# Kernel tuning notes

Measured on AMD Instinct MI355X. Metric: run time of the kernel, lower is better.

The kernel has to match this reference:

```python
import jax, jax.numpy as jnp
import numpy as np

N_TOKENS = 32768
INPUT_DIM = 1024
HIDDEN_DIM = 256
NUM_EXPERTS = 64
TOP_K = 2


def setup_inputs() -> dict:
    key = jax.random.key(0)
    kx, k1, k2, kb1, kb2 = jax.random.split(key, 5)
    # torch nn.Linear init scale ~ U(-1/sqrt(fan_in), 1/sqrt(fan_in)); use small normals
    x = jax.random.normal(kx, (N_TOKENS, INPUT_DIM), dtype=jnp.float32)
    w1 = jax.random.normal(k1, (HIDDEN_DIM, INPUT_DIM), dtype=jnp.float32) / np.sqrt(INPUT_DIM)
    b1 = jax.random.normal(kb1, (HIDDEN_DIM,), dtype=jnp.float32) * 0.01
    w2 = jax.random.normal(k2, (NUM_EXPERTS, HIDDEN_DIM), dtype=jnp.float32) / np.sqrt(HIDDEN_DIM)
    b2 = jax.random.normal(kb2, (NUM_EXPERTS,), dtype=jnp.float32) * 0.01
    return {"x": x, "w1": w1, "b1": b1, "w2": w2, "b2": b2}


def reference(x, w1, b1, w2, b2):
    # logits = Linear -> ReLU -> Linear
    h = jax.nn.relu(jnp.einsum("nd,hd->nh", x, w1) + b1)       # [N, hidden]
    logits = jnp.einsum("nh,eh->ne", h, w2) + b2               # [N, experts]
    top_k_logits, top_k_indices = jax.lax.top_k(logits, TOP_K)  # [N, k]
    top_k_gates = jax.nn.softmax(top_k_logits, axis=-1)
    return top_k_indices, top_k_gates
```

## Files before the change

### kernel.cpp

```cpp
#include <hip/hip_runtime.h>
#include <math.h>

#define N_TOK 32768
#define IN_DIM 1024
#define HID 256
#define NE 64

__global__ __launch_bounds__(256, 2)
void gemm1_relu(const float* __restrict__ x, const float* __restrict__ w1,
                const float* __restrict__ b1, float* __restrict__ h)
{
    __shared__ float Xs[32][72];
    __shared__ float Ws[32][256];

    const int tid = threadIdx.x;
    const int t0  = blockIdx.x * 64;
    const int tg  = tid >> 5;
    const int hg  = tid & 31;

    float acc[8][8];
    #pragma unroll
    for (int i = 0; i < 8; ++i)
        #pragma unroll
        for (int j = 0; j < 8; ++j) acc[i][j] = 0.f;

    for (int k0 = 0; k0 < IN_DIM; k0 += 32) {
        #pragma unroll
        for (int r = 0; r < 2; ++r) {
            int slot = tid + 256 * r;
            int t  = slot >> 3;
            int kq = (slot & 7) * 4;
            float4 v = *(const float4*)(x + (size_t)(t0 + t) * IN_DIM + k0 + kq);
            Xs[kq + 0][t] = v.x; Xs[kq + 1][t] = v.y;
            Xs[kq + 2][t] = v.z; Xs[kq + 3][t] = v.w;
        }
        #pragma unroll
        for (int r = 0; r < 8; ++r) {
            int slot = tid + 256 * r;
            int hh = slot >> 3;
            int kq = (slot & 7) * 4;
            float4 v = *(const float4*)(w1 + (size_t)hh * IN_DIM + k0 + kq);
            Ws[kq + 0][hh] = v.x; Ws[kq + 1][hh] = v.y;
            Ws[kq + 2][hh] = v.z; Ws[kq + 3][hh] = v.w;
        }
        __syncthreads();

        #pragma unroll
        for (int k = 0; k < 32; ++k) {
            float xv[8], wv[8];
            *(float4*)&xv[0] = *(const float4*)&Xs[k][tg * 8];
            *(float4*)&xv[4] = *(const float4*)&Xs[k][tg * 8 + 4];
            *(float4*)&wv[0] = *(const float4*)&Ws[k][hg * 8];
            *(float4*)&wv[4] = *(const float4*)&Ws[k][hg * 8 + 4];
            #pragma unroll
            for (int i = 0; i < 8; ++i)
                #pragma unroll
                for (int j = 0; j < 8; ++j)
                    acc[i][j] = fmaf(xv[i], wv[j], acc[i][j]);
        }
        __syncthreads();
    }

    float4 bv0 = *(const float4*)(b1 + hg * 8);
    float4 bv1 = *(const float4*)(b1 + hg * 8 + 4);
    float bias[8] = {bv0.x, bv0.y, bv0.z, bv0.w, bv1.x, bv1.y, bv1.z, bv1.w};
    #pragma unroll
    for (int i = 0; i < 8; ++i) {
        int t = t0 + tg * 8 + i;
        float4 o0, o1;
        o0.x = fmaxf(acc[i][0] + bias[0], 0.f);
        o0.y = fmaxf(acc[i][1] + bias[1], 0.f);
        o0.z = fmaxf(acc[i][2] + bias[2], 0.f);
        o0.w = fmaxf(acc[i][3] + bias[3], 0.f);
        o1.x = fmaxf(acc[i][4] + bias[4], 0.f);
        o1.y = fmaxf(acc[i][5] + bias[5], 0.f);
        o1.z = fmaxf(acc[i][6] + bias[6], 0.f);
        o1.w = fmaxf(acc[i][7] + bias[7], 0.f);
        *(float4*)(h + (size_t)t * HID + hg * 8)     = o0;
        *(float4*)(h + (size_t)t * HID + hg * 8 + 4) = o1;
    }
}

__global__ __launch_bounds__(256, 2)
void gemm2_topk(const float* __restrict__ h, const float* __restrict__ w2,
                const float* __restrict__ b2, float* __restrict__ out)
{
    __shared__ float Hs[32][72];
    __shared__ float W2s[32][64];
    __shared__ float Ls[64][65];

    const int tid = threadIdx.x;
    const int t0  = blockIdx.x * 64;
    const int tg  = tid >> 4;
    const int eg  = tid & 15;

    float acc[4][4];
    #pragma unroll
    for (int i = 0; i < 4; ++i)
        #pragma unroll
        for (int j = 0; j < 4; ++j) acc[i][j] = 0.f;

    for (int k0 = 0; k0 < HID; k0 += 32) {
        #pragma unroll
        for (int r = 0; r < 2; ++r) {
            int slot = tid + 256 * r;
            int t  = slot >> 3;
            int kq = (slot & 7) * 4;
            float4 v = *(const float4*)(h + (size_t)(t0 + t) * HID + k0 + kq);
            Hs[kq + 0][t] = v.x; Hs[kq + 1][t] = v.y;
            Hs[kq + 2][t] = v.z; Hs[kq + 3][t] = v.w;
        }
        #pragma unroll
        for (int r = 0; r < 2; ++r) {
            int slot = tid + 256 * r;
            int e  = slot >> 3;
            int kq = (slot & 7) * 4;
            float4 v = *(const float4*)(w2 + (size_t)e * HID + k0 + kq);
            W2s[kq + 0][e] = v.x; W2s[kq + 1][e] = v.y;
            W2s[kq + 2][e] = v.z; W2s[kq + 3][e] = v.w;
        }
        __syncthreads();

        #pragma unroll
        for (int k = 0; k < 32; ++k) {
            float hv[4], wv[4];
            *(float4*)&hv[0] = *(const float4*)&Hs[k][tg * 4];
            *(float4*)&wv[0] = *(const float4*)&W2s[k][eg * 4];
            #pragma unroll
            for (int i = 0; i < 4; ++i)
                #pragma unroll
                for (int j = 0; j < 4; ++j)
                    acc[i][j] = fmaf(hv[i], wv[j], acc[i][j]);
        }
        __syncthreads();
    }

    float4 b2v = *(const float4*)(b2 + eg * 4);
    float bb[4] = {b2v.x, b2v.y, b2v.z, b2v.w};
    #pragma unroll
    for (int i = 0; i < 4; ++i)
        #pragma unroll
        for (int j = 0; j < 4; ++j)
            Ls[tg * 4 + i][eg * 4 + j] = acc[i][j] + bb[j];
    __syncthreads();

    if (tid < 64) {
        const int t = tid;
        float m1 = -INFINITY, m2 = -INFINITY;
        int i1 = 0, i2 = 0;
        #pragma unroll 8
        for (int e = 0; e < NE; ++e) {
            float v = Ls[t][e];
            if (v > m1) { m2 = m1; i2 = i1; m1 = v; i1 = e; }
            else if (v > m2) { m2 = v; i2 = e; }
        }
        float e2  = expf(m2 - m1);
        float inv = 1.f / (1.f + e2);
        float g1  = inv;
        float g2  = e2 * inv;
        int gt = t0 + t;
        out[(size_t)gt * 2 + 0] = (float)i1;
        out[(size_t)gt * 2 + 1] = (float)i2;
        out[(size_t)2 * N_TOK + (size_t)gt * 2 + 0] = g1;
        out[(size_t)2 * N_TOK + (size_t)gt * 2 + 1] = g2;
    }
}

extern "C" void kernel_launch(void* const* d_in, const int* in_sizes, int n_in,
                              void* d_out, int out_size, void* d_ws, size_t ws_size,
                              hipStream_t stream) {
    const float* x  = (const float*)d_in[0];
    const float* w1 = (const float*)d_in[1];
    const float* b1 = (const float*)d_in[2];
    const float* w2 = (const float*)d_in[3];
    const float* b2 = (const float*)d_in[4];
    float* out = (float*)d_out;
    float* h   = (float*)d_ws;

    gemm1_relu<<<N_TOK / 64, 256, 0, stream>>>(x, w1, b1, h);
    gemm2_topk<<<N_TOK / 64, 256, 0, stream>>>(h, w2, b2, out);
}
```

Measured before the change: 417.8 us.

## Fuse both gating GEMMs and top-k into one kernel with swizzled LDS and prefetch

After: 556.4 us. 33.2% more time.

```diff
diff --git a/kernel.cpp b/kernel.cpp
--- a/kernel.cpp
+++ b/kernel.cpp
@@ -6,12 +6,18 @@
 #define HID 256
 #define NE 64
 
+union SMem {
+    struct { float Xs[32][64]; float Ws[32][256]; } a;
+    struct { float Hs[128][64]; float W2s[32][64]; } b;
+    float Ls[64][67];
+};
+
 __global__ __launch_bounds__(256, 2)
-void gemm1_relu(const float* __restrict__ x, const float* __restrict__ w1,
-                const float* __restrict__ b1, float* __restrict__ h)
+void moe_gate_fused(const float* __restrict__ x,  const float* __restrict__ w1,
+                    const float* __restrict__ b1, const float* __restrict__ w2,
+                    const float* __restrict__ b2, float* __restrict__ out)
 {
-    __shared__ float Xs[32][72];
-    __shared__ float Ws[32][256];
+    __shared__ SMem sm;
 
     const int tid = threadIdx.x;
     const int t0  = blockIdx.x * 64;
@@ -24,124 +30,162 @@
         #pragma unroll
         for (int j = 0; j < 8; ++j) acc[i][j] = 0.f;
 
-    for (int k0 = 0; k0 < IN_DIM; k0 += 32) {
+    float4 px[2], pw[8];
+    #pragma unroll
+    for (int r = 0; r < 2; ++r) {
+        int slot = tid + 256 * r;
+        int t = slot >> 3, kq = (slot & 7) * 4;
+        px[r] = *(const float4*)(x + (size_t)(t0 + t) * IN_DIM + kq);
+    }
+    #pragma unroll
+    for (int r = 0; r < 8; ++r) {
+        int slot = tid + 256 * r;
+        int hh = slot >> 3, kq = (slot & 7) * 4;
+        pw[r] = *(const float4*)(w1 + (size_t)hh * IN_DIM + kq);
+    }
+
+    #pragma unroll 1
+    for (int c = 0; c < 32; ++c) {
         #pragma unroll
         for (int r = 0; r < 2; ++r) {
             int slot = tid + 256 * r;
-            int t  = slot >> 3;
-            int kq = (slot & 7) * 4;
-            float4 v = *(const float4*)(x + (size_t)(t0 + t) * IN_DIM + k0 + kq);
-            Xs[kq + 0][t] = v.x; Xs[kq + 1][t] = v.y;
-            Xs[kq + 2][t] = v.z; Xs[kq + 3][t] = v.w;
+            int t = slot >> 3, kq = (slot & 7) * 4;
+            int col = (((t >> 2) ^ (kq >> 2)) << 2) | (t & 3);
+            sm.a.Xs[kq + 0][col] = px[r].x;
+            sm.a.Xs[kq + 1][col] = px[r].y;
+            sm.a.Xs[kq + 2][col] = px[r].z;
+            sm.a.Xs[kq + 3][col] = px[r].w;
         }
         #pragma unroll
         for (int r = 0; r < 8; ++r) {
             int slot = tid + 256 * r;
-            int hh = slot >> 3;
-            int kq = (slot & 7) * 4;
-            float4 v = *(const float4*)(w1 + (size_t)hh * IN_DIM + k0 + kq);
-            Ws[kq + 0][hh] = v.x; Ws[kq + 1][hh] = v.y;
-            Ws[kq + 2][hh] = v.z; Ws[kq + 3][hh] = v.w;
+            int hh = slot >> 3, kq = (slot & 7) * 4;
+            int col = (((hh >> 2) ^ (kq >> 2)) << 2) | (hh & 3);
+            sm.a.Ws[kq + 0][col] = pw[r].x;
+            sm.a.Ws[kq + 1][col] = pw[r].y;
+            sm.a.Ws[kq + 2][col] = pw[r].z;
+            sm.a.Ws[kq + 3][col] = pw[r].w;
         }
         __syncthreads();
 
-        #pragma unroll
-        for (int k = 0; k < 32; ++k) {
-            float xv[8], wv[8];
-            *(float4*)&xv[0] = *(const float4*)&Xs[k][tg * 8];
-            *(float4*)&xv[4] = *(const float4*)&Xs[k][tg * 8 + 4];
-            *(float4*)&wv[0] = *(const float4*)&Ws[k][hg * 8];
-            *(float4*)&wv[4] = *(const float4*)&Ws[k][hg * 8 + 4];
-            #pragma unroll
-            for (int i = 0; i < 8; ++i)
+        if (c < 31) {
+            int k0 = (c + 1) * 32;
+            #pragma unroll
+            for (int r = 0; r < 2; ++r) {
+                int slot = tid + 256 * r;
+                int t = slot >> 3, kq = (slot & 7) * 4;
+                px[r] = *(const float4*)(x + (size_t)(t0 + t) * IN_DIM + k0 + kq);
+            }
+            #pragma unroll
+            for (int r = 0; r < 8; ++r) {
+                int slot = tid + 256 * r;
+                int hh = slot >> 3, kq = (slot & 7) * 4;
+                pw[r] = *(const float4*)(w1 + (size_t)hh * IN_DIM + k0 + kq);
+            }
+        }
+
+        #pragma unroll
+        for (int m = 0; m < 8; ++m) {
+            const float* xb0 = &sm.a.Xs[0][(((tg * 2)     ^ m) << 2)];
+            const float* xb1 = &sm.a.Xs[0][(((tg * 2 + 1) ^ m) << 2)];
+            const float* wb0 = &sm.a.Ws[0][(( hg ^ m)        << 2)];
+            const float* wb1 = &sm.a.Ws[0][((((hg ^ m) + 32)) << 2)];
+            #pragma unroll
+            for (int kk = 0; kk < 4; ++kk) {
+                int k = m * 4 + kk;
+                float4 xv0 = *(const float4*)(xb0 + k * 64);
+                float4 xv1 = *(const float4*)(xb1 + k * 64);
+                float4 wv0 = *(const float4*)(wb0 + k * 256);
+                float4 wv1 = *(const float4*)(wb1 + k * 256);
+                float xv[8] = {xv0.x, xv0.y, xv0.z, xv0.w, xv1.x, xv1.y, xv1.z, xv1.w};
+                float wv[8] = {wv0.x, wv0.y, wv0.z, wv0.w, wv1.x, wv1.y, wv1.z, wv1.w};
                 #pragma unroll
-                for (int j = 0; j < 8; ++j)
-                    acc[i][j] = fmaf(xv[i], wv[j], acc[i][j]);
+                for (int i = 0; i < 8; ++i)
+                    #pragma unroll
+                    for (int j = 0; j < 8; ++j)
+                        acc[i][j] = fmaf(xv[i], wv[j], acc[i][j]);
+            }
         }
         __syncthreads();
     }
 
-    float4 bv0 = *(const float4*)(b1 + hg * 8);
-    float4 bv1 = *(const float4*)(b1 + hg * 8 + 4);
-    float bias[8] = {bv0.x, bv0.y, bv0.z, bv0.w, bv1.x, bv1.y, bv1.z, bv1.w};
-    #pragma unroll
-    for (int i = 0; i < 8; ++i) {
-        int t = t0 + tg * 8 + i;
-        float4 o0, o1;
-        o0.x = fmaxf(acc[i][0] + bias[0], 0.f);
-        o0.y = fmaxf(acc[i][1] + bias[1], 0.f);
-        o0.z = fmaxf(acc[i][2] + bias[2], 0.f);
-        o0.w = fmaxf(acc[i][3] + bias[3], 0.f);
-        o1.x = fmaxf(acc[i][4] + bias[4], 0.f);
-        o1.y = fmaxf(acc[i][5] + bias[5], 0.f);
-        o1.z = fmaxf(acc[i][6] + bias[6], 0.f);
-        o1.w = fmaxf(acc[i][7] + bias[7], 0.f);
-        *(float4*)(h + (size_t)t * HID + hg * 8)     = o0;
-        *(float4*)(h + (size_t)t * HID + hg * 8 + 4) = o1;
-    }
-}
-
-__global__ __launch_bounds__(256, 2)
-void gemm2_topk(const float* __restrict__ h, const float* __restrict__ w2,
-                const float* __restrict__ b2, float* __restrict__ out)
-{
-    __shared__ float Hs[32][72];
-    __shared__ float W2s[32][64];
-    __shared__ float Ls[64][65];
-
-    const int tid = threadIdx.x;
-    const int t0  = blockIdx.x * 64;
-    const int tg  = tid >> 4;
-    const int eg  = tid & 15;
-
-    float acc[4][4];
+    {
+        float4 bb0 = *(const float4*)(b1 + hg * 4);
+        float4 bb1 = *(const float4*)(b1 + 128 + hg * 4);
+        float bias1[8] = {bb0.x, bb0.y, bb0.z, bb0.w, bb1.x, bb1.y, bb1.z, bb1.w};
+        #pragma unroll
+        for (int i = 0; i < 8; ++i)
+            #pragma unroll
+            for (int j = 0; j < 8; ++j)
+                acc[i][j] = fmaxf(acc[i][j] + bias1[j], 0.f);
+    }
+
+    const int ta = tid >> 4;
+    const int eb = tid & 15;
+
+    float acc2[4][4];
     #pragma unroll
     for (int i = 0; i < 4; ++i)
         #pragma unroll
-        for (int j = 0; j < 4; ++j) acc[i][j] = 0.f;
-
-    for (int k0 = 0; k0 < HID; k0 += 32) {
-        #pragma unroll
-        for (int r = 0; r < 2; ++r) {
-            int slot = tid + 256 * r;
-            int t  = slot >> 3;
-            int kq = (slot & 7) * 4;
-            float4 v = *(const float4*)(h + (size_t)(t0 + t) * HID + k0 + kq);
-            Hs[kq + 0][t] = v.x; Hs[kq + 1][t] = v.y;
-            Hs[kq + 2][t] = v.z; Hs[kq + 3][t] = v.w;
-        }
-        #pragma unroll
-        for (int r = 0; r < 2; ++r) {
-            int slot = tid + 256 * r;
-            int e  = slot >> 3;
-            int kq = (slot & 7) * 4;
-            float4 v = *(const float4*)(w2 + (size_t)e * HID + k0 + kq);
-            W2s[kq + 0][e] = v.x; W2s[kq + 1][e] = v.y;
-            W2s[kq + 2][e] = v.z; W2s[kq + 3][e] = v.w;
-        }
-        __syncthreads();
-
-        #pragma unroll
-        for (int k = 0; k < 32; ++k) {
-            float hv[4], wv[4];
-            *(float4*)&hv[0] = *(const float4*)&Hs[k][tg * 4];
-            *(float4*)&wv[0] = *(const float4*)&W2s[k][eg * 4];
-            #pragma unroll
-            for (int i = 0; i < 4; ++i)
+        for (int j = 0; j < 4; ++j) acc2[i][j] = 0.f;
+
+    #pragma unroll
+    for (int p = 0; p < 2; ++p) {
+        #pragma unroll
+        for (int i = 0; i < 8; ++i) {
+            int t = tg * 8 + i;
+            int col = (((t >> 2) ^ (hg & 15)) << 2) | (t & 3);
+            #pragma unroll
+            for (int jj = 0; jj < 4; ++jj) {
+                int hl = hg * 4 + jj;
+                sm.b.Hs[hl][col] = acc[i][p * 4 + jj];
+            }
+        }
+        #pragma unroll 1
+        for (int c4 = 0; c4 < 4; ++c4) {
+            #pragma unroll
+            for (int r = 0; r < 2; ++r) {
+                int slot = tid + 256 * r;
+                int e = slot >> 3, kq = (slot & 7) * 4;
+                float4 v = *(const float4*)(w2 + (size_t)e * HID + p * 128 + c4 * 32 + kq);
+                int col = (((e >> 2) ^ (kq >> 2)) << 2) | (e & 3);
+                sm.b.W2s[kq + 0][col] = v.x;
+                sm.b.W2s[kq + 1][col] = v.y;
+                sm.b.W2s[kq + 2][col] = v.z;
+                sm.b.W2s[kq + 3][col] = v.w;
+            }
+            __syncthreads();
+            #pragma unroll
+            for (int m = 0; m < 8; ++m) {
+                const float* wb = &sm.b.W2s[0][((eb ^ m) << 2)];
                 #pragma unroll
-                for (int j = 0; j < 4; ++j)
-                    acc[i][j] = fmaf(hv[i], wv[j], acc[i][j]);
-        }
-        __syncthreads();
-    }
-
-    float4 b2v = *(const float4*)(b2 + eg * 4);
-    float bb[4] = {b2v.x, b2v.y, b2v.z, b2v.w};
-    #pragma unroll
-    for (int i = 0; i < 4; ++i)
-        #pragma unroll
-        for (int j = 0; j < 4; ++j)
-            Ls[tg * 4 + i][eg * 4 + j] = acc[i][j] + bb[j];
+                for (int kk = 0; kk < 4; ++kk) {
+                    int k  = m * 4 + kk;
+                    int hl = c4 * 32 + k;
+                    float4 hv = *(const float4*)&sm.b.Hs[hl][((ta ^ ((hl >> 2) & 15)) << 2)];
+                    float4 wv = *(const float4*)(wb + k * 64);
+                    float hvv[4] = {hv.x, hv.y, hv.z, hv.w};
+                    float wvv[4] = {wv.x, wv.y, wv.z, wv.w};
+                    #pragma unroll
+                    for (int i = 0; i < 4; ++i)
+                        #pragma unroll
+                        for (int j = 0; j < 4; ++j)
+                            acc2[i][j] = fmaf(hvv[i], wvv[j], acc2[i][j]);
+                }
+            }
+            __syncthreads();
+        }
+    }
+
+    {
+        float4 b2v = *(const float4*)(b2 + eb * 4);
+        float bb2[4] = {b2v.x, b2v.y, b2v.z, b2v.w};
+        #pragma unroll
+        for (int i = 0; i < 4; ++i)
+            #pragma unroll
+            for (int j = 0; j < 4; ++j)
+                sm.Ls[ta * 4 + i][eb * 4 + j] = acc2[i][j] + bb2[j];
+    }
     __syncthreads();
 
     if (tid < 64) {
@@ -150,19 +194,17 @@
         int i1 = 0, i2 = 0;
         #pragma unroll 8
         for (int e = 0; e < NE; ++e) {
-            float v = Ls[t][e];
-            if (v > m1) { m2 = m1; i2 = i1; m1 = v; i1 = e; }
+            float v = sm.Ls[t][e];
+            if (v > m1)      { m2 = m1; i2 = i1; m1 = v; i1 = e; }
             else if (v > m2) { m2 = v; i2 = e; }
         }
         float e2  = expf(m2 - m1);
         float inv = 1.f / (1.f + e2);
-        float g1  = inv;
-        float g2  = e2 * inv;
         int gt = t0 + t;
         out[(size_t)gt * 2 + 0] = (float)i1;
         out[(size_t)gt * 2 + 1] = (float)i2;
-        out[(size_t)2 * N_TOK + (size_t)gt * 2 + 0] = g1;
-        out[(size_t)2 * N_TOK + (size_t)gt * 2 + 1] = g2;
+        out[(size_t)2 * N_TOK + (size_t)gt * 2 + 0] = inv;
+        out[(size_t)2 * N_TOK + (size_t)gt * 2 + 1] = e2 * inv;
     }
 }
 
@@ -175,8 +217,6 @@
     const float* w2 = (const float*)d_in[3];
     const float* b2 = (const float*)d_in[4];
     float* out = (float*)d_out;
-    float* h   = (float*)d_ws;
-
-    gemm1_relu<<<N_TOK / 64, 256, 0, stream>>>(x, w1, b1, h);
-    gemm2_topk<<<N_TOK / 64, 256, 0, stream>>>(h, w2, b2, out);
+
+    moe_gate_fused<<<N_TOK / 64, 256, 0, stream>>>(x, w1, b1, w2, b2, out);
 }
```
